# Kernel optimization log

Measured on AMD Instinct MI355X. Metric: run time of the kernel, lower is better.

## Reference

```python
import jax, jax.numpy as jnp
import numpy as np

B, T, V, E, H, L = 64, 512, 256, 1024, 1024, 2


def setup_inputs() -> dict:
    key = jax.random.key(0)
    ks = jax.random.split(key, 9)
    s = 1.0 / np.sqrt(H)
    X = jax.random.randint(ks[0], (B, T), 0, V)
    h0 = jax.random.uniform(ks[1], (L, B, H), dtype=jnp.float32)
    emb = (jax.random.normal(ks[2], (V, E), dtype=jnp.float32) * 0.02).at[0].set(0.0)  # pad_idx=0 row zeroed
    W_ih = jax.random.normal(ks[3], (L, 3 * H, H), dtype=jnp.float32) * s
    W_hh = jax.random.normal(ks[4], (L, 3 * H, H), dtype=jnp.float32) * s
    b_ih = jax.random.normal(ks[5], (L, 3 * H), dtype=jnp.float32) * s
    b_hh = jax.random.normal(ks[6], (L, 3 * H), dtype=jnp.float32) * s
    W_out = jax.random.normal(ks[7], (V, H), dtype=jnp.float32) * s
    b_out = jax.random.normal(ks[8], (V,), dtype=jnp.float32) * s
    return {"X": X, "h0": h0, "emb": emb, "W_ih": W_ih, "W_hh": W_hh,
            "b_ih": b_ih, "b_hh": b_hh, "W_out": W_out, "b_out": b_out}


def _gru_layer(x, h0_l, W_ih_l, W_hh_l, b_ih_l, b_hh_l):
    # x: [B, T, D]; PyTorch GRU cell math (gate order r, z, n).
    gx = jnp.einsum('btd,gd->btg', x, W_ih_l) + b_ih_l  # [B, T, 3H], precomputed input GEMM

    def step(h, gx_t):  # gx_t: [B, 3H]
        gh = h @ W_hh_l.T + b_hh_l
        xr, xz, xn = jnp.split(gx_t, 3, axis=-1)
        hr, hz, hn = jnp.split(gh, 3, axis=-1)
        r = jax.nn.sigmoid(xr + hr)
        z = jax.nn.sigmoid(xz + hz)
        n = jnp.tanh(xn + r * hn)
        h_new = (1.0 - z) * n + z * h
        return h_new, h_new

    _, ys = jax.lax.scan(step, h0_l, jnp.swapaxes(gx, 0, 1))  # scan over time
    return jnp.swapaxes(ys, 0, 1)  # [B, T, H]


def reference(X, h0, emb, W_ih, W_hh, b_ih, b_hh, W_out, b_out):
    # Embedding lookup (dropout is identity in eval mode)
    x = emb[X]  # [B, T, E]
    for l in range(L):
        x = _gru_layer(x, h0[l], W_ih[l], W_hh[l], b_ih[l], b_hh[l])
    logits = jnp.einsum('bth,vh->btv', x, W_out) + b_out  # [B, T, V]
    # fptt returns out[:, :-1].reshape(-1, token_count)
    return logits[:, :-1, :].reshape(-1, V)
```

## Files before the change

kernel.cpp:

```cpp
#include <hip/hip_runtime.h>
#include <stdint.h>


namespace {

constexpr int B = 64, T = 512, V = 256, H = 1024, G = 3072;
constexpr int NWRK = 192;
constexpr int NBLK = NWRK + 3;
constexpr int SLAB = 65536;
constexpr int R1MASK = 127;

typedef _Float16 f16;
typedef unsigned long long u64;
typedef f16 f16x8 __attribute__((ext_vector_type(8)));
typedef f16 f16x4 __attribute__((ext_vector_type(4)));
typedef float f32x4 __attribute__((ext_vector_type(4)));

#define MFMA16(av, bv, acc) __builtin_amdgcn_mfma_f32_16x16x32_f16(av, bv, acc, 0, 0, 0)

__device__ __forceinline__ f16x8 lload16(const f16* p) {
  return *reinterpret_cast<const f16x8*>(p);
}
__device__ __forceinline__ float lload2(const f16* p) { return (float)*p; }

__device__ __forceinline__ void astore2(f16* p, float v) {
  union { f16 f; unsigned short s; } u;
  u.f = (f16)v;
  __hip_atomic_store(reinterpret_cast<unsigned short*>(p), u.s,
                     __ATOMIC_RELAXED, __HIP_MEMORY_SCOPE_AGENT);
}
__device__ __forceinline__ float aloadf(const float* p) {
  return __hip_atomic_load(p, __ATOMIC_RELAXED, __HIP_MEMORY_SCOPE_AGENT);
}
__device__ __forceinline__ void astoref(float* p, float v) {
  __hip_atomic_store(p, v, __ATOMIC_RELAXED, __HIP_MEMORY_SCOPE_AGENT);
}
__device__ __forceinline__ void astorei(int* p, int v) {
  __hip_atomic_store(p, v, __ATOMIC_RELAXED, __HIP_MEMORY_SCOPE_AGENT);
}
__device__ __forceinline__ int aloadi(const int* p) {
  return __hip_atomic_load(p, __ATOMIC_RELAXED, __HIP_MEMORY_SCOPE_AGENT);
}
__device__ __forceinline__ void waitge(const int* p, int target) {
  while (aloadi(p) < target) __builtin_amdgcn_s_sleep(1);
}

__device__ __forceinline__ void mm48(const f16* a, const f16* wp, f32x4& aR,
                                     f32x4& aZ, f32x4& aN) {
  f16x8 ring[8];
#pragma unroll
  for (int q = 0; q < 8; ++q) ring[q] = lload16(a + q * 2048);
#pragma unroll
  for (int k0 = 0; k0 < 32; ++k0) {
    f16x8 av = ring[k0 & 7];
    if (k0 + 8 < 32) ring[k0 & 7] = lload16(a + (k0 + 8) * 2048);
    const f16* w = wp + k0 * 1728;
    aR = MFMA16(av, *reinterpret_cast<const f16x8*>(w), aR);
    aZ = MFMA16(av, *reinterpret_cast<const f16x8*>(w + 576), aZ);
    aN = MFMA16(av, *reinterpret_cast<const f16x8*>(w + 1152), aN);
  }
}

__global__ void to_f16_4(const float* __restrict__ src, f16* __restrict__ dst,
                         int n4) {
  int i = blockIdx.x * 256 + threadIdx.x;
  if (i >= n4) return;
  float4 v = reinterpret_cast<const float4*>(src)[i];
  f16x4 o = {(f16)v.x, (f16)v.y, (f16)v.z, (f16)v.w};
  reinterpret_cast<f16x4*>(dst)[i] = o;
}

__global__ void pack_w(const float* __restrict__ Whh,
                       const float* __restrict__ Wih, f16* __restrict__ dst) {
  const int id = blockIdx.x * 256 + threadIdx.x;
  const int kkq = id & 3;
  const int rr = id >> 2;
  const int row = rr % 48;
  const int rest = rr / 48;
  const int k0 = rest & 31, bi = (rest >> 5) & 63, which = rest >> 11;
  const int g = row >> 4, jrow = row & 15;
  const float* base = (which == 0) ? Whh
                    : (which == 1) ? (Wih + (size_t)G * H)
                                   : (Whh + (size_t)G * H);
  const float* src =
      base + ((size_t)(g * H + bi * 16 + jrow)) * H + k0 * 32 + kkq * 8;
  float4 a = *reinterpret_cast<const float4*>(src);
  float4 b = *reinterpret_cast<const float4*>(src + 4);
  f16x8 o = {(f16)a.x, (f16)a.y, (f16)a.z, (f16)a.w,
             (f16)b.x, (f16)b.y, (f16)b.z, (f16)b.w};
  *reinterpret_cast<f16x8*>(dst + (size_t)id * 8) = o;
}

__global__ void pack_h0f(const float* __restrict__ h0, f16* __restrict__ h1r,
                         f16* __restrict__ h2r, int* __restrict__ bar) {
  if (blockIdx.x == 0 && threadIdx.x < NWRK) {
    const int t4 = threadIdx.x * 16;
    bar[t4] = 0;
    bar[4096 + t4] = 0;
    bar[8192 + t4] = 0;
    bar[12288 + t4] = 0;
  }
  const int id = blockIdx.x * 256 + threadIdx.x;
  const int layer = id >> 16, b = (id >> 10) & 63, j = id & 1023;
  const size_t a = ((size_t)(j >> 5) * 64 + b) * 32 + (j & 31);
  const f16 v = (f16)h0[id];
  if (layer == 0) h1r[a] = v; else h2r[a] = v;
}

template <int MODE>
__global__ __launch_bounds__(256) void gemm_f16(
    const f16* __restrict__ A, const f16* __restrict__ Bm,
    const float* __restrict__ bias, float* __restrict__ C, int M, int N,
    int K) {
  __shared__ __align__(16) f16 As[64][48], Bs[64][48];

  const int tid = threadIdx.x;
  const int lane = tid & 63, wv = tid >> 6;
  const int bm = blockIdx.y, bn = blockIdx.x;
  const int srow = tid >> 2, sseg = (tid & 3) * 8;

  const f16* pA = (MODE == 2)
                      ? (A + (size_t)bm * 65536 + srow * 32 + sseg)
                      : (A + (size_t)(bm * 64 + srow) * K + sseg);
  const f16* pB = Bm + (size_t)(bn * 64 + srow) * K + sseg;

  f32x4 acc[4];
  const f32x4 zero = {0.f, 0.f, 0.f, 0.f};
#pragma unroll
  for (int nt = 0; nt < 4; ++nt) acc[nt] = zero;

  const int ar = wv * 16 + (lane & 15);
  const int kk = (lane >> 4) * 8;

  const int niter = K / 32;
  for (int ki = 0; ki < niter; ++ki) {
    int4 va = (MODE == 2) ? *reinterpret_cast<const int4*>(pA + ki * 2048)
                          : *reinterpret_cast<const int4*>(pA + ki * 32);
    int4 vb = *reinterpret_cast<const int4*>(pB + ki * 32);
    __syncthreads();
    *reinterpret_cast<int4*>(&As[srow][sseg]) = va;
    *reinterpret_cast<int4*>(&Bs[srow][sseg]) = vb;
    __syncthreads();

    f16x8 av = *reinterpret_cast<const f16x8*>(&As[ar][kk]);
#pragma unroll
    for (int nt = 0; nt < 4; ++nt) {
      f16x8 bv = *reinterpret_cast<const f16x8*>(&Bs[nt * 16 + (lane & 15)][kk]);
      acc[nt] = MFMA16(av, bv, acc[nt]);
    }
  }

  const int rbase = wv * 16 + (lane >> 4) * 4;
  const int cl = lane & 15;
#pragma unroll
  for (int nt = 0; nt < 4; ++nt) {
    const int n = bn * 64 + nt * 16 + cl;
    const float bv = bias[n];
#pragma unroll
    for (int r = 0; r < 4; ++r) {
      const int m = bm * 64 + rbase + r;
      const float v = acc[nt][r] + bv;
      if (MODE == 0) {
        C[(size_t)m * N + n] = v;
      } else {
        const int t = m >> 6, bb = m & 63;
        if (t < T - 1) C[((size_t)(bb * (T - 1) + t)) * V + n] = v;
      }
    }
  }
}

__global__ __launch_bounds__(256, 1) void gru_persist(
    const f16* __restrict__ pW, const float* __restrict__ G0,
    const int* __restrict__ X, const float* __restrict__ b_hh,
    const float* __restrict__ b_ih, f16* __restrict__ h1ring,
    f16* __restrict__ h2ring, float* __restrict__ gx2, int* __restrict__ bar) {
  __shared__ __align__(16) f16 Wt[55296];

  const int tid = threadIdx.x, bx = blockIdx.x;

  int* arrive = bar;

  if (bx >= NWRK) {
    const int r = bx - NWRK;
    if (tid < 64) {
      const int* slot = arrive + (r * 64 + tid) * 16;
      int* dr = bar + 4096 * (1 + r);
      const int lo = r + 1;
      const int hi = (r == 0) ? 512 : 513;
      int ph = lo;
      while (ph <= hi) {
        int m;
        for (;;) {
          m = aloadi(slot);
#pragma unroll
          for (int o = 32; o; o >>= 1) {
            int t2 = __shfl_xor(m, o, 64);
            m = m < t2 ? m : t2;
          }
          if (m >= ph) break;
        }
        if (m > hi) m = hi;
        astorei(&dr[tid * 16], m);
        astorei(&dr[(64 + tid) * 16], m);
        astorei(&dr[(128 + tid) * 16], m);
        ph = m + 1;
      }
    }
    return;
  }

  const int lane = tid & 63, wv = tid >> 6;
  const int l15 = lane & 15, kq = lane >> 4;
  const int role = bx >> 6, jb = bx & 63;

  const int* door0 = bar + 4096 + bx * 16;
  const int* door1 = bar + 8192 + bx * 16;
  const int* door2 = bar + 12288 + bx * 16;

  {
    const int2* src = reinterpret_cast<const int2*>(pW + (size_t)bx * 49152);
#pragma unroll
    for (int q = 0; q < 48; ++q) {
      const int flat = q * 256 + tid;
      const int k0r = flat >> 3, seg = flat & 7;
      *reinterpret_cast<int2*>(&Wt[k0r * 36 + seg * 4]) = src[flat];
    }
  }
  __syncthreads();

  const int j = jb * 16 + l15;
  float br_ = 0.f, bz_ = 0.f, bn_ = 0.f, bxr_ = 0.f, bxz_ = 0.f, bxn_ = 0.f;
  if (role == 0) {
    br_ = b_hh[j]; bz_ = b_hh[H + j]; bn_ = b_hh[2 * H + j];
  } else if (role == 2) {
    br_ = b_hh[G + j]; bz_ = b_hh[G + H + j]; bn_ = b_hh[G + 2 * H + j];
    bxr_ = b_ih[G + j]; bxz_ = b_ih[G + H + j]; bxn_ = b_ih[G + 2 * H + j];
  }

  const int aoff = (wv * 16 + l15) * 32 + kq * 8;
  const f16* wp = Wt + l15 * 36 + kq * 8;
  const int bB = wv * 16 + kq * 4;
  const size_t hoff = (size_t)(j >> 5) * 2048 + (j & 31);

  const int i0 = (role == 0) ? 0 : (role == 1) ? 1 : 2;
  const int i1 = (role == 0) ? (T - 1) : (role == 1) ? T : (T + 1);

  for (int i = i0; i <= i1; ++i) {
    if (tid == 0) {
      if (role == 0) {
        if (i >= 1) waitge(door0, i);
        if (i >= 128) waitge(door1, i - 126);
      } else if (role == 1) {
        waitge(door0, i);
        if (i >= 9) waitge(door2, i - 6);
      } else {
        waitge(door1, i);
        if (i > 2) waitge(door2, i);
      }
    }
    __syncthreads();

    if (role == 0) {
      const f16* hin = h1ring + (size_t)(i & R1MASK) * SLAB;
      f16* hout = h1ring + (size_t)((i + 1) & R1MASK) * SLAB;
      f32x4 aR = {0, 0, 0, 0}, aZ = {0, 0, 0, 0}, aN = {0, 0, 0, 0};
      mm48(hin + aoff, wp, aR, aZ, aN);
#pragma unroll
      for (int r = 0; r < 4; ++r) {
        const int b = bB + r;
        const float* gx = G0 + (size_t)X[b * T + i] * G;
        const float xr = gx[j], xz = gx[H + j], xn = gx[2 * H + j];
        const size_t ha = hoff + (size_t)b * 32;
        const float hp = lload2(hin + ha);
        const float rg = 1.f / (1.f + __expf(-(xr + aR[r] + br_)));
        const float zg = 1.f / (1.f + __expf(-(xz + aZ[r] + bz_)));
        const float ng = tanhf(xn + rg * (aN[r] + bn_));
        astore2(hout + ha, (1.f - zg) * ng + zg * hp);
      }
    } else if (role == 1) {
      const int t = i - 1;
      f32x4 aR = {0, 0, 0, 0}, aZ = {0, 0, 0, 0}, aN = {0, 0, 0, 0};
      mm48(h1ring + (size_t)(i & R1MASK) * SLAB + aoff, wp, aR, aZ, aN);
      float* gdst = gx2 + ((size_t)((t & 7) * 64 + jb)) * 3072;
#pragma unroll
      for (int r = 0; r < 4; ++r) {
        const int b = bB + r;
        astoref(gdst + b * 16 + l15, aR[r]);
        astoref(gdst + 1024 + b * 16 + l15, aZ[r]);
        astoref(gdst + 2048 + b * 16 + l15, aN[r]);
      }
    } else {
      const int t = i - 2;
      const f16* hin = h2ring + (size_t)t * SLAB;
      f16* hout = h2ring + (size_t)(t + 1) * SLAB;
      const float* gsrc = gx2 + ((size_t)((t & 7) * 64 + jb)) * 3072;
      f32x4 aR = {0, 0, 0, 0}, aZ = {0, 0, 0, 0}, aN = {0, 0, 0, 0};
      mm48(hin + aoff, wp, aR, aZ, aN);
#pragma unroll
      for (int r = 0; r < 4; ++r) {
        const int b = bB + r;
        const float xr = aloadf(gsrc + b * 16 + l15);
        const float xz = aloadf(gsrc + 1024 + b * 16 + l15);
        const float xn = aloadf(gsrc + 2048 + b * 16 + l15);
        const size_t ha = hoff + (size_t)b * 32;
        const float hp = lload2(hin + ha);
        const float rg = 1.f / (1.f + __expf(-(xr + bxr_ + aR[r] + br_)));
        const float zg = 1.f / (1.f + __expf(-(xz + bxz_ + aZ[r] + bz_)));
        const float ng = tanhf(xn + bxn_ + rg * (aN[r] + bn_));
        const float hv = (1.f - zg) * ng + zg * hp;
        astore2(hout + ha, hv);
      }
    }

    asm volatile("s_waitcnt vmcnt(0)" ::: "memory");
    __builtin_amdgcn_sched_barrier(0);
    __syncthreads();
    if (tid == 0) astorei(&arrive[bx * 16], i + 1);
  }
}

}

extern "C" void kernel_launch(void* const* d_in, const int* in_sizes, int n_in,
                              void* d_out, int out_size, void* d_ws,
                              size_t ws_size, hipStream_t stream) {
  const int* X = (const int*)d_in[0];
  const float* h0 = (const float*)d_in[1];
  const float* emb = (const float*)d_in[2];
  const float* W_ih = (const float*)d_in[3];
  const float* W_hh = (const float*)d_in[4];
  const float* b_ih = (const float*)d_in[5];
  const float* b_hh = (const float*)d_in[6];
  const float* W_out = (const float*)d_in[7];
  const float* b_out = (const float*)d_in[8];
  float* out = (float*)d_out;
  (void)in_sizes; (void)n_in; (void)out_size; (void)ws_size;

  char* p = (char*)d_ws;
  auto alloc = [&](size_t bytes) {
    char* q = p;
    p += (bytes + 255) & ~(size_t)255;
    return q;
  };
  f16* pW = (f16*)alloc((size_t)3 * 64 * 49152 * 2);
  float* G0 = (float*)alloc((size_t)V * G * 4);
  f16* emb16 = (f16*)alloc((size_t)V * H * 2);
  f16* wih0_16 = (f16*)alloc((size_t)G * H * 2);
  f16* wout16 = (f16*)alloc((size_t)V * H * 2);
  f16* h1ring = (f16*)alloc((size_t)128 * 65536 * 2);
  f16* h2ring = (f16*)alloc((size_t)513 * 65536 * 2);
  float* gx2 = (float*)alloc((size_t)8 * 64 * 3072 * 4);
  int* bar = (int*)alloc(65536);

  to_f16_4<<<(V * H / 4 + 255) / 256, 256, 0, stream>>>(emb, emb16, V * H / 4);
  to_f16_4<<<(G * H / 4 + 255) / 256, 256, 0, stream>>>(W_ih, wih0_16,
                                                        G * H / 4);
  to_f16_4<<<(V * H / 4 + 255) / 256, 256, 0, stream>>>(W_out, wout16,
                                                        V * H / 4);
  pack_w<<<4608, 256, 0, stream>>>(W_hh, W_ih, pW);
  pack_h0f<<<512, 256, 0, stream>>>(h0, h1ring, h2ring, bar);
  gemm_f16<0><<<dim3(G / 64, V / 64), 256, 0, stream>>>(emb16, wih0_16, b_ih,
                                                        G0, V, G, H);

  {
    const f16* a0 = pW; const float* a1 = G0; const int* a2 = X;
    const float* a3 = b_hh; const float* a4 = b_ih;
    f16* a5 = h1ring; f16* a6 = h2ring; float* a7 = gx2; int* a8 = bar;
    void* args[] = {&a0, &a1, &a2, &a3, &a4, &a5, &a6, &a7, &a8};
    hipLaunchCooperativeKernel((const void*)gru_persist, dim3(NBLK), dim3(256),
                               args, 0, stream);
  }

  gemm_f16<2><<<dim3(V / 64, T), 256, 0, stream>>>(h2ring + 65536, wout16,
                                                   b_out, out, T * B, V, H);
}
```

Before: 7.654 ms.

## Replace aggregator-block barrier with direct per-wave polling of arrival slots

Removes the three extra aggregator blocks that min-reduced per-block arrival counters and republished them as per-block doors. Each worker block now has its first two waves poll the 64 producer arrive slots directly, one lane per slot, before the block sync. This drops one hop of cross-block latency per step on the recurrent critical path. In exchange every consumer block polls 64 slots itself, which adds L2/atomic traffic and contention.

```diff
diff --git a/kernel.cpp b/kernel.cpp
--- a/kernel.cpp
+++ b/kernel.cpp
@@ -5,8 +5,7 @@
 namespace {
 
 constexpr int B = 64, T = 512, V = 256, H = 1024, G = 3072;
-constexpr int NWRK = 192;
-constexpr int NBLK = NWRK + 3;
+constexpr int NBLK = 192;
 constexpr int SLAB = 65536;
 constexpr int R1MASK = 127;
 
@@ -93,12 +92,8 @@
 
 __global__ void pack_h0f(const float* __restrict__ h0, f16* __restrict__ h1r,
                          f16* __restrict__ h2r, int* __restrict__ bar) {
-  if (blockIdx.x == 0 && threadIdx.x < NWRK) {
-    const int t4 = threadIdx.x * 16;
-    bar[t4] = 0;
-    bar[4096 + t4] = 0;
-    bar[8192 + t4] = 0;
-    bar[12288 + t4] = 0;
+  if (blockIdx.x == 0 && threadIdx.x < NBLK) {
+    bar[threadIdx.x * 16] = 0;
   }
   const int id = blockIdx.x * 256 + threadIdx.x;
   const int layer = id >> 16, b = (id >> 10) & 63, j = id & 1023;
@@ -178,45 +173,11 @@
   __shared__ __align__(16) f16 Wt[55296];
 
   const int tid = threadIdx.x, bx = blockIdx.x;
-
-  int* arrive = bar;
-
-  if (bx >= NWRK) {
-    const int r = bx - NWRK;
-    if (tid < 64) {
-      const int* slot = arrive + (r * 64 + tid) * 16;
-      int* dr = bar + 4096 * (1 + r);
-      const int lo = r + 1;
-      const int hi = (r == 0) ? 512 : 513;
-      int ph = lo;
-      while (ph <= hi) {
-        int m;
-        for (;;) {
-          m = aloadi(slot);
-#pragma unroll
-          for (int o = 32; o; o >>= 1) {
-            int t2 = __shfl_xor(m, o, 64);
-            m = m < t2 ? m : t2;
-          }
-          if (m >= ph) break;
-        }
-        if (m > hi) m = hi;
-        astorei(&dr[tid * 16], m);
-        astorei(&dr[(64 + tid) * 16], m);
-        astorei(&dr[(128 + tid) * 16], m);
-        ph = m + 1;
-      }
-    }
-    return;
-  }
-
   const int lane = tid & 63, wv = tid >> 6;
   const int l15 = lane & 15, kq = lane >> 4;
   const int role = bx >> 6, jb = bx & 63;
 
-  const int* door0 = bar + 4096 + bx * 16;
-  const int* door1 = bar + 8192 + bx * 16;
-  const int* door2 = bar + 12288 + bx * 16;
+  int* arrive = bar;
 
   {
     const int2* src = reinterpret_cast<const int2*>(pW + (size_t)bx * 49152);
@@ -247,16 +208,22 @@
   const int i1 = (role == 0) ? (T - 1) : (role == 1) ? T : (T + 1);
 
   for (int i = i0; i <= i1; ++i) {
-    if (tid == 0) {
+    if (tid < 64) {
       if (role == 0) {
-        if (i >= 1) waitge(door0, i);
-        if (i >= 128) waitge(door1, i - 126);
+        if (i >= 1) waitge(&arrive[(0 * 64 + tid) * 16], i);
       } else if (role == 1) {
-        waitge(door0, i);
-        if (i >= 9) waitge(door2, i - 6);
+        waitge(&arrive[(0 * 64 + tid) * 16], i);
       } else {
-        waitge(door1, i);
-        if (i > 2) waitge(door2, i);
+        waitge(&arrive[(1 * 64 + tid) * 16], i);
+      }
+    } else if (tid < 128) {
+      const int l = tid - 64;
+      if (role == 0) {
+        if (i >= 128) waitge(&arrive[(1 * 64 + l) * 16], i - 126);
+      } else if (role == 1) {
+        if (i >= 9) waitge(&arrive[(2 * 64 + l) * 16], i - 6);
+      } else {
+        if (i > 2) waitge(&arrive[(2 * 64 + l) * 16], i);
       }
     }
     __syncthreads();
```

Measured after the change: 7.369 ms. -3.7%, faster.
